# Optimization experiments

Measured on AMD Instinct MI355X. Metric: run time of the kernel, lower is better.

## Reference

```python
import jax, jax.numpy as jnp
import numpy as np

DIMS = 1024
HEAD = 16
HEAD_DIM = DIMS // HEAD  # 64
BASE_THETA = 10000.0


def setup_inputs() -> dict:
    key = jax.random.key(0)
    ks = jax.random.split(key, 8)
    B, S = 2, 2048
    x = jax.random.normal(ks[0], (B, S, DIMS), dtype=jnp.float32)
    # causal additive mask (use -1e9 instead of -inf for finite grads)
    mask = jnp.where(jnp.tril(jnp.ones((S, S), dtype=bool)), 0.0, -1e9).astype(jnp.float32)
    init = 0.02
    Wq = jax.random.normal(ks[1], (DIMS, DIMS), dtype=jnp.float32) * init
    bq = jnp.zeros((DIMS,), dtype=jnp.float32)
    Wk = jax.random.normal(ks[2], (DIMS, DIMS), dtype=jnp.float32) * init  # no bias
    Wv = jax.random.normal(ks[3], (DIMS, DIMS), dtype=jnp.float32) * init
    bv = jnp.zeros((DIMS,), dtype=jnp.float32)
    Wo = jax.random.normal(ks[4], (DIMS, DIMS), dtype=jnp.float32) * init
    bo = jnp.zeros((DIMS,), dtype=jnp.float32)
    # learned rotary frequencies, initialized exactly as the torch module
    inv_freq = (1.0 / (BASE_THETA ** (jnp.arange(0, HEAD_DIM, 2, dtype=jnp.float32) / HEAD_DIM))).astype(jnp.float32)
    return {"x": x, "mask": mask, "Wq": Wq, "bq": bq, "Wk": Wk, "Wv": Wv,
            "bv": bv, "Wo": Wo, "bo": bo, "inv_freq": inv_freq}


def _apply_rotary(x, cos, sin):
    # x: [B,H,S,D] with D == 2 * len(inv_freq); cos/sin: [S, D/2]
    xr = x.reshape(*x.shape[:-1], -1, 2)  # [B,H,S,D/2,2]
    a, b = xr[..., 0], xr[..., 1]
    ra = a * cos - b * sin
    rb = a * sin + b * cos
    return jnp.stack([ra, rb], axis=-1).reshape(x.shape)


def reference(x, mask, Wq, bq, Wk, Wv, bv, Wo, bo, inv_freq):
    B, S, D = x.shape
    H, hd = HEAD, HEAD_DIM
    q = jnp.einsum('bsd,ed->bse', x, Wq) + bq
    k = jnp.einsum('bsd,ed->bse', x, Wk)
    v = jnp.einsum('bsd,ed->bse', x, Wv) + bv
    # [B,S,D] -> [B,H,S,hd]
    q = q.reshape(B, S, H, hd).transpose(0, 2, 1, 3)
    k = k.reshape(B, S, H, hd).transpose(0, 2, 1, 3)
    v = v.reshape(B, S, H, hd).transpose(0, 2, 1, 3)
    # rotary embeddings (complex mul expressed with cos/sin)
    t = jnp.arange(S, dtype=jnp.float32)
    freqs = t[:, None] * inv_freq[None, :]  # [S, hd/2]
    cos, sin = jnp.cos(freqs), jnp.sin(freqs)
    q = _apply_rotary(q, cos, sin)
    k = _apply_rotary(k, cos, sin)
    scale = hd ** (-0.25)
    qk = jnp.einsum('bhqd,bhkd->bhqk', q * scale, k * scale)
    qk = qk + mask[:S, :S]
    qk = qk.astype(jnp.float32)
    w = jax.nn.softmax(qk, axis=-1)  # dropout is identity in eval mode
    out = jnp.einsum('bhqk,bhkd->bhqd', w, v)
    out = out.transpose(0, 2, 1, 3).reshape(B, S, D)
    out = jnp.einsum('bsd,ed->bse', out, Wo) + bo
    return (out, qk)
```

## Files before the change

kernel.cpp:

```cpp
#include <hip/hip_runtime.h>

typedef __attribute__((ext_vector_type(8))) short short8;
typedef __attribute__((ext_vector_type(4))) float floatx4;
typedef unsigned short ushort_t;

static __device__ __forceinline__ ushort_t f2bf(float f) {
  union { float f; unsigned u; } v; v.f = f;
  unsigned r = v.u + 0x7fffu + ((v.u >> 16) & 1u);
  return (ushort_t)(r >> 16);
}
static __device__ __forceinline__ float bf2f(ushort_t s) {
  union { unsigned u; float f; } v; v.u = ((unsigned)s) << 16; return v.f;
}

#define L2E 1.4426950408889634f

__global__ void conv_kernel(const float* __restrict__ src, ushort_t* __restrict__ dst, int n) {
  int i = (blockIdx.x * blockDim.x + threadIdx.x) * 4;
  if (i >= n) return;
  float4 f = *(const float4*)(src + i);
  ushort4 u;
  u.x = f2bf(f.x); u.y = f2bf(f.y); u.z = f2bf(f.z); u.w = f2bf(f.w);
  *(ushort4*)(dst + i) = u;
}

__global__ void biascat_kernel(const float* __restrict__ bq, const float* __restrict__ bv,
                               float* __restrict__ bcat) {
  int i = blockIdx.x * blockDim.x + threadIdx.x;
  float v = 0.f;
  if (i < 1024) v = bq[i];
  else if (i >= 2048) v = bv[i - 2048];
  bcat[i] = v;
}

__global__ __launch_bounds__(256) void gemm_bt(
    const ushort_t* __restrict__ A, const ushort_t* __restrict__ Bm,
    const float* __restrict__ bias, float* __restrict__ Cf,
    ushort_t* __restrict__ Cb, int M, int N, int K)
{
  __shared__ ushort_t As[128 * 72];
  __shared__ ushort_t Bs[128 * 72];
  const int tid = threadIdx.x;
  const int wave = tid >> 6, lane = tid & 63;
  const int wm = wave >> 1, wn = wave & 1;
  const int lane15 = lane & 15, quad = lane >> 4;
  const int m0 = blockIdx.y * 128, n0 = blockIdx.x * 128;
  const int lrow = tid >> 3;
  const int lcol = (tid & 7) * 8;

  floatx4 acc[4][4];
#pragma unroll
  for (int a = 0; a < 4; ++a)
#pragma unroll
    for (int b = 0; b < 4; ++b) acc[a][b] = (floatx4){0.f, 0.f, 0.f, 0.f};

  for (int k0 = 0; k0 < K; k0 += 64) {
    __syncthreads();
#pragma unroll
    for (int l = 0; l < 4; ++l) {
      int row = l * 32 + lrow;
      *(short8*)(&As[row * 72 + lcol]) = *(const short8*)(A + (size_t)(m0 + row) * K + k0 + lcol);
      *(short8*)(&Bs[row * 72 + lcol]) = *(const short8*)(Bm + (size_t)(n0 + row) * K + k0 + lcol);
    }
    __syncthreads();
#pragma unroll
    for (int ks = 0; ks < 64; ks += 32) {
      short8 af[4], bf[4];
#pragma unroll
      for (int mi = 0; mi < 4; ++mi)
        af[mi] = *(const short8*)(&As[(wm * 64 + mi * 16 + lane15) * 72 + ks + quad * 8]);
#pragma unroll
      for (int ni = 0; ni < 4; ++ni)
        bf[ni] = *(const short8*)(&Bs[(wn * 64 + ni * 16 + lane15) * 72 + ks + quad * 8]);
#pragma unroll
      for (int mi = 0; mi < 4; ++mi)
#pragma unroll
        for (int ni = 0; ni < 4; ++ni)
          acc[mi][ni] = __builtin_amdgcn_mfma_f32_16x16x32_bf16(af[mi], bf[ni], acc[mi][ni], 0, 0, 0);
    }
  }

#pragma unroll
  for (int mi = 0; mi < 4; ++mi) {
#pragma unroll
    for (int ni = 0; ni < 4; ++ni) {
      const int col = n0 + wn * 64 + ni * 16 + lane15;
      const float bv = bias ? bias[col] : 0.f;
#pragma unroll
      for (int v = 0; v < 4; ++v) {
        const int row = m0 + wm * 64 + mi * 16 + quad * 4 + v;
        const float val = acc[mi][ni][v] + bv;
        if (Cf) Cf[(size_t)row * N + col] = val;
        else    Cb[(size_t)row * N + col] = f2bf(val);
      }
    }
  }
}

__global__ void rotary_kernel(ushort_t* __restrict__ qkv, const float* __restrict__ inv_freq,
                              int colbase) {
  int tid = blockIdx.x * blockDim.x + threadIdx.x;
  int f = tid & 31;
  int h = (tid >> 5) & 15;
  int s = (tid >> 9) & 2047;
  int b = tid >> 20;
  size_t idx = (size_t)(b * 2048 + s) * 3072 + colbase + h * 64 + 2 * f;
  float ang = (float)s * inv_freq[f];
  float sn, cs;
  sincosf(ang, &sn, &cs);
  float a = bf2f(qkv[idx]);
  float bb = bf2f(qkv[idx + 1]);
  qkv[idx]     = f2bf(a * cs - bb * sn);
  qkv[idx + 1] = f2bf(a * sn + bb * cs);
}

__global__ void transpose_v_kernel(const ushort_t* __restrict__ QKV, ushort_t* __restrict__ VtG) {
  int g = blockIdx.x * blockDim.x + threadIdx.x;
  int s = g & 2047;
  int dchunk = (g >> 11) & 7;
  int bh = g >> 14;
  int b = bh >> 4, h = bh & 15;
  short8 v = *(const short8*)(QKV + (size_t)(b * 2048 + s) * 3072 + 2048 + h * 64 + dchunk * 8);
  ushort_t* dst = VtG + (size_t)bh * 64 * 2048 + (size_t)dchunk * 8 * 2048 + s;
#pragma unroll
  for (int e = 0; e < 8; ++e) dst[(size_t)e * 2048] = (ushort_t)v[e];
}

__global__ void fill_kernel(float* __restrict__ qk_out) {
  const int tile = blockIdx.x;
  const int it = tile >> 4, jt = tile & 15;
  if (jt <= it) return;
  const float4 val = {-1e9f, -1e9f, -1e9f, -1e9f};
  float* base = qk_out + (size_t)blockIdx.y * 2048 * 2048 + (size_t)it * 128 * 2048 + jt * 128;
#pragma unroll
  for (int l = 0; l < 16; ++l) {
    int idx = l * 256 + threadIdx.x;
    int row = idx >> 5, c4 = (idx & 31) * 4;
    *(float4*)(base + (size_t)row * 2048 + c4) = val;
  }
}

__global__ __launch_bounds__(256) void score_kernel(
    const ushort_t* __restrict__ QKV, float* __restrict__ qk_out,
    float2* __restrict__ pstats )
{
  const int tid = threadIdx.x;
  const int w = tid >> 6, lane = tid & 63;
  const int lane15 = lane & 15, quad = lane >> 4;
  const int t = blockIdx.x;
  const int bh = blockIdx.y;
  const int b = bh >> 4, h = bh & 15;

  int it = (int)((sqrtf((float)(8 * t + 1)) - 1.0f) * 0.5f);
  while ((it + 1) * (it + 2) / 2 <= t) ++it;
  while (it * (it + 1) / 2 > t) --it;
  const int jt = t - it * (it + 1) / 2;

  const int i_base = it * 128 + w * 32;
  const int j0 = jt * 128;
  const size_t srow0 = (size_t)b * 2048;

  short8 aq[2][2];
#pragma unroll
  for (int mi = 0; mi < 2; ++mi)
#pragma unroll
    for (int kb = 0; kb < 2; ++kb)
      aq[mi][kb] = *(const short8*)(QKV + (srow0 + i_base + mi * 16 + lane15) * 3072
                                    + h * 64 + kb * 32 + quad * 8);

  floatx4 s[2][8];
#pragma unroll
  for (int mi = 0; mi < 2; ++mi)
#pragma unroll
    for (int ni = 0; ni < 8; ++ni) s[mi][ni] = (floatx4){0.f, 0.f, 0.f, 0.f};
#pragma unroll
  for (int ni = 0; ni < 8; ++ni) {
#pragma unroll
    for (int kb = 0; kb < 2; ++kb) {
      short8 bk = *(const short8*)(QKV + (srow0 + j0 + ni * 16 + lane15) * 3072
                                   + 1024 + h * 64 + kb * 32 + quad * 8);
      s[0][ni] = __builtin_amdgcn_mfma_f32_16x16x32_bf16(aq[0][kb], bk, s[0][ni], 0, 0, 0);
      s[1][ni] = __builtin_amdgcn_mfma_f32_16x16x32_bf16(aq[1][kb], bk, s[1][ni], 0, 0, 0);
    }
  }

  float* qk_bh = qk_out + (size_t)bh * 2048 * 2048;

#pragma unroll
  for (int mi = 0; mi < 2; ++mi) {
#pragma unroll
    for (int ni = 0; ni < 8; ++ni) {
      const int j_g = j0 + ni * 16 + lane15;
#pragma unroll
      for (int v = 0; v < 4; ++v) {
        const int i_g = i_base + mi * 16 + quad * 4 + v;
        float val = s[mi][ni][v] * 0.125f + ((j_g <= i_g) ? 0.f : -1e9f);
        s[mi][ni][v] = val;
        qk_bh[(size_t)i_g * 2048 + j_g] = val;
      }
    }
  }

#pragma unroll
  for (int mi = 0; mi < 2; ++mi) {
#pragma unroll
    for (int v = 0; v < 4; ++v) {
      float mv = -3.0e38f;
#pragma unroll
      for (int ni = 0; ni < 8; ++ni) mv = fmaxf(mv, s[mi][ni][v]);
#pragma unroll
      for (int off = 1; off < 16; off <<= 1)
        mv = fmaxf(mv, __shfl_xor(mv, off));
      float ls = 0.f;
#pragma unroll
      for (int ni = 0; ni < 8; ++ni)
        ls += exp2f((s[mi][ni][v] - mv) * L2E);
#pragma unroll
      for (int off = 1; off < 16; off <<= 1)
        ls += __shfl_xor(ls, off);
      if (lane15 == 0) {
        const int i_g = i_base + mi * 16 + quad * 4 + v;
        pstats[(size_t)(bh * 2048 + i_g) * 16 + jt] = make_float2(mv, ls);
      }
    }
  }
}

__global__ void stats_kernel(const float2* __restrict__ pstats, float2* __restrict__ fstats) {
  int r = blockIdx.x * blockDim.x + threadIdx.x;
  int i = r & 2047;
  int nt = (i >> 7) + 1;
  const float2* p = pstats + (size_t)r * 16;
  float m = -3.0e38f;
  for (int t = 0; t < nt; ++t) m = fmaxf(m, p[t].x);
  float l = 0.f;
  for (int t = 0; t < nt; ++t) l += p[t].y * exp2f((p[t].x - m) * L2E);
  fstats[r] = make_float2(m, 1.f / l);
}

__global__ __launch_bounds__(256) void pv_kernel(
    const float* __restrict__ qk, const ushort_t* __restrict__ VtG,
    const float2* __restrict__ fstats, ushort_t* __restrict__ AO)
{
  const int tid = threadIdx.x;
  const int w = tid >> 6, lane = tid & 63;
  const int lane15 = lane & 15, quad = lane >> 4;
  const int wid = blockIdx.x * 4 + w;
  const int bh = wid >> 6, p = wid & 63;
  const int b = bh >> 4, h = bh & 15;

  const float* qk_bh = qk + (size_t)bh * 2048 * 2048;
  const ushort_t* Vt_bh = VtG + (size_t)bh * 64 * 2048;
  const float2* fs = fstats + (size_t)bh * 2048;

#pragma unroll
  for (int half = 0; half < 2; ++half) {
    const int s16 = half ? (127 - p) : p;
    const int i0 = s16 * 16;
    const int njt = (s16 >> 3) + 1;
    const float mr = fs[i0 + lane15].x;

    floatx4 o[4];
#pragma unroll
    for (int nd = 0; nd < 4; ++nd) o[nd] = (floatx4){0.f, 0.f, 0.f, 0.f};

    for (int jt = 0; jt < njt; ++jt) {
      const int j0 = jt * 128;
      const float* srow = qk_bh + (size_t)(i0 + lane15) * 2048 + j0 + quad * 8;

      short8 ap[4];
#pragma unroll
      for (int kb = 0; kb < 4; ++kb) {
        float4 a0 = *(const float4*)(srow + kb * 32);
        float4 a1 = *(const float4*)(srow + kb * 32 + 4);
        short8 a;
        a[0] = (short)f2bf(exp2f((a0.x - mr) * L2E));
        a[1] = (short)f2bf(exp2f((a0.y - mr) * L2E));
        a[2] = (short)f2bf(exp2f((a0.z - mr) * L2E));
        a[3] = (short)f2bf(exp2f((a0.w - mr) * L2E));
        a[4] = (short)f2bf(exp2f((a1.x - mr) * L2E));
        a[5] = (short)f2bf(exp2f((a1.y - mr) * L2E));
        a[6] = (short)f2bf(exp2f((a1.z - mr) * L2E));
        a[7] = (short)f2bf(exp2f((a1.w - mr) * L2E));
        ap[kb] = a;
      }

#pragma unroll
      for (int kb = 0; kb < 4; ++kb)
#pragma unroll
        for (int nd = 0; nd < 4; ++nd) {
          short8 bv = *(const short8*)(Vt_bh + (size_t)(nd * 16 + lane15) * 2048
                                       + j0 + kb * 32 + quad * 8);
          o[nd] = __builtin_amdgcn_mfma_f32_16x16x32_bf16(ap[kb], bv, o[nd], 0, 0, 0);
        }
    }

    float inv[4];
#pragma unroll
    for (int v = 0; v < 4; ++v) inv[v] = fs[i0 + quad * 4 + v].y;
#pragma unroll
    for (int nd = 0; nd < 4; ++nd)
#pragma unroll
      for (int v = 0; v < 4; ++v) {
        const int i_g = i0 + quad * 4 + v;
        AO[((size_t)b * 2048 + i_g) * 1024 + h * 64 + nd * 16 + lane15] =
            f2bf(o[nd][v] * inv[v]);
      }
  }
}

extern "C" void kernel_launch(void* const* d_in, const int* in_sizes, int n_in,
                              void* d_out, int out_size, void* d_ws, size_t ws_size,
                              hipStream_t stream) {
  const float* x  = (const float*)d_in[0];
  const float* Wq = (const float*)d_in[2];
  const float* bq = (const float*)d_in[3];
  const float* Wk = (const float*)d_in[4];
  const float* Wv = (const float*)d_in[5];
  const float* bv = (const float*)d_in[6];
  const float* Wo = (const float*)d_in[7];
  const float* bo = (const float*)d_in[8];
  const float* inv_freq = (const float*)d_in[9];

  char* ws = (char*)d_ws;
  ushort_t* xb   = (ushort_t*)(ws);
  ushort_t* vtg  = (ushort_t*)(ws);
  ushort_t* wb   = (ushort_t*)(ws + ((size_t)8  << 20));
  float*    bcat = (float*)   (ws + ((size_t)16 << 20));
  float2*   fstats = (float2*)(ws + ((size_t)16 << 20));
  ushort_t* qkv  = (ushort_t*)(ws + ((size_t)17 << 20));
  float2*   pstats = (float2*)(ws + ((size_t)41 << 20));
  ushort_t* aob  = (ushort_t*)(ws + ((size_t)41 << 20));

  float* out0  = (float*)d_out;
  float* qkout = out0 + 4194304;

  conv_kernel<<<4096, 256, 0, stream>>>(x, xb, 4194304);
  conv_kernel<<<1024, 256, 0, stream>>>(Wq, wb,           1048576);
  conv_kernel<<<1024, 256, 0, stream>>>(Wk, wb + 1048576, 1048576);
  conv_kernel<<<1024, 256, 0, stream>>>(Wv, wb + 2097152, 1048576);
  conv_kernel<<<1024, 256, 0, stream>>>(Wo, wb + 3145728, 1048576);
  biascat_kernel<<<12, 256, 0, stream>>>(bq, bv, bcat);

  gemm_bt<<<dim3(24, 32), 256, 0, stream>>>(xb, wb, bcat, nullptr, qkv, 4096, 3072, 1024);

  rotary_kernel<<<8192, 256, 0, stream>>>(qkv, inv_freq, 0);
  rotary_kernel<<<8192, 256, 0, stream>>>(qkv, inv_freq, 1024);

  transpose_v_kernel<<<2048, 256, 0, stream>>>(qkv, vtg);

  fill_kernel<<<dim3(256, 32), 256, 0, stream>>>(qkout);

  score_kernel<<<dim3(136, 32), 256, 0, stream>>>(qkv, qkout, pstats);

  stats_kernel<<<256, 256, 0, stream>>>(pstats, fstats);

  pv_kernel<<<512, 256, 0, stream>>>(qkout, vtg, fstats, aob);

  gemm_bt<<<dim3(8, 32), 256, 0, stream>>>(aob, wb + 3145728, bo, out0, nullptr, 4096, 1024, 1024);
}
```

Before: 949.2 us.

## Use direct global-to-LDS loads in GEMM and split PV key tiles across wave pairs

The GEMM tile loads now use global_load_lds to copy from global memory straight into LDS, dropping the register round-trip. The LDS rows lose their padding (stride 64 instead of 72), which may add bank conflicts on the MFMA fragment reads. The PV kernel now gives each row-pair to two waves that handle alternating key tiles, then combines their partial accumulators through shared memory. This doubles the launched blocks to improve occupancy and latency hiding in the memory-bound PV pass, at the cost of an LDS reduction and a block barrier.

```diff
diff --git a/kernel.cpp b/kernel.cpp
--- a/kernel.cpp
+++ b/kernel.cpp
@@ -3,6 +3,9 @@
 typedef __attribute__((ext_vector_type(8))) short short8;
 typedef __attribute__((ext_vector_type(4))) float floatx4;
 typedef unsigned short ushort_t;
+
+typedef __attribute__((address_space(1))) const ushort_t gas_ushort;
+typedef __attribute__((address_space(3))) ushort_t las_ushort;
 
 static __device__ __forceinline__ ushort_t f2bf(float f) {
   union { float f; unsigned u; } v; v.f = f;
@@ -38,15 +41,15 @@
     const float* __restrict__ bias, float* __restrict__ Cf,
     ushort_t* __restrict__ Cb, int M, int N, int K)
 {
-  __shared__ ushort_t As[128 * 72];
-  __shared__ ushort_t Bs[128 * 72];
+  __shared__ ushort_t As[128 * 64];
+  __shared__ ushort_t Bs[128 * 64];
   const int tid = threadIdx.x;
   const int wave = tid >> 6, lane = tid & 63;
   const int wm = wave >> 1, wn = wave & 1;
   const int lane15 = lane & 15, quad = lane >> 4;
   const int m0 = blockIdx.y * 128, n0 = blockIdx.x * 128;
-  const int lrow = tid >> 3;
-  const int lcol = (tid & 7) * 8;
+  const int srow = lane >> 3;
+  const int scol = (lane & 7) * 8;
 
   floatx4 acc[4][4];
 #pragma unroll
@@ -57,10 +60,15 @@
   for (int k0 = 0; k0 < K; k0 += 64) {
     __syncthreads();
 #pragma unroll
-    for (int l = 0; l < 4; ++l) {
-      int row = l * 32 + lrow;
-      *(short8*)(&As[row * 72 + lcol]) = *(const short8*)(A + (size_t)(m0 + row) * K + k0 + lcol);
-      *(short8*)(&Bs[row * 72 + lcol]) = *(const short8*)(Bm + (size_t)(n0 + row) * K + k0 + lcol);
+    for (int pc = 0; pc < 4; ++pc) {
+      const int chunk = pc * 4 + wave;
+      const int row = chunk * 8 + srow;
+      __builtin_amdgcn_global_load_lds(
+          (gas_ushort*)(A + (size_t)(m0 + row) * K + k0 + scol),
+          (las_ushort*)(As + chunk * 512 + lane * 8), 16, 0, 0);
+      __builtin_amdgcn_global_load_lds(
+          (gas_ushort*)(Bm + (size_t)(n0 + row) * K + k0 + scol),
+          (las_ushort*)(Bs + chunk * 512 + lane * 8), 16, 0, 0);
     }
     __syncthreads();
 #pragma unroll
@@ -68,10 +76,10 @@
       short8 af[4], bf[4];
 #pragma unroll
       for (int mi = 0; mi < 4; ++mi)
-        af[mi] = *(const short8*)(&As[(wm * 64 + mi * 16 + lane15) * 72 + ks + quad * 8]);
+        af[mi] = *(const short8*)(&As[(wm * 64 + mi * 16 + lane15) * 64 + ks + quad * 8]);
 #pragma unroll
       for (int ni = 0; ni < 4; ++ni)
-        bf[ni] = *(const short8*)(&Bs[(wn * 64 + ni * 16 + lane15) * 72 + ks + quad * 8]);
+        bf[ni] = *(const short8*)(&Bs[(wn * 64 + ni * 16 + lane15) * 64 + ks + quad * 8]);
 #pragma unroll
       for (int mi = 0; mi < 4; ++mi)
 #pragma unroll
@@ -242,16 +250,24 @@
     const float* __restrict__ qk, const ushort_t* __restrict__ VtG,
     const float2* __restrict__ fstats, ushort_t* __restrict__ AO)
 {
+  __shared__ float cbuf[2][2][4][64][4];
   const int tid = threadIdx.x;
   const int w = tid >> 6, lane = tid & 63;
   const int lane15 = lane & 15, quad = lane >> 4;
-  const int wid = blockIdx.x * 4 + w;
-  const int bh = wid >> 6, p = wid & 63;
+  const int pib = w >> 1, sub = w & 1;
+  const int pairId = blockIdx.x * 2 + pib;
+  const int bh = pairId >> 6, p = pairId & 63;
   const int b = bh >> 4, h = bh & 15;
 
   const float* qk_bh = qk + (size_t)bh * 2048 * 2048;
   const ushort_t* Vt_bh = VtG + (size_t)bh * 64 * 2048;
   const float2* fs = fstats + (size_t)bh * 2048;
+
+  floatx4 o[2][4];
+#pragma unroll
+  for (int half = 0; half < 2; ++half)
+#pragma unroll
+    for (int nd = 0; nd < 4; ++nd) o[half][nd] = (floatx4){0.f, 0.f, 0.f, 0.f};
 
 #pragma unroll
   for (int half = 0; half < 2; ++half) {
@@ -260,11 +276,7 @@
     const int njt = (s16 >> 3) + 1;
     const float mr = fs[i0 + lane15].x;
 
-    floatx4 o[4];
-#pragma unroll
-    for (int nd = 0; nd < 4; ++nd) o[nd] = (floatx4){0.f, 0.f, 0.f, 0.f};
-
-    for (int jt = 0; jt < njt; ++jt) {
+    for (int jt = sub; jt < njt; jt += 2) {
       const int j0 = jt * 128;
       const float* srow = qk_bh + (size_t)(i0 + lane15) * 2048 + j0 + quad * 8;
 
@@ -291,21 +303,38 @@
         for (int nd = 0; nd < 4; ++nd) {
           short8 bv = *(const short8*)(Vt_bh + (size_t)(nd * 16 + lane15) * 2048
                                        + j0 + kb * 32 + quad * 8);
-          o[nd] = __builtin_amdgcn_mfma_f32_16x16x32_bf16(ap[kb], bv, o[nd], 0, 0, 0);
+          o[half][nd] = __builtin_amdgcn_mfma_f32_16x16x32_bf16(ap[kb], bv, o[half][nd], 0, 0, 0);
         }
     }
-
-    float inv[4];
-#pragma unroll
-    for (int v = 0; v < 4; ++v) inv[v] = fs[i0 + quad * 4 + v].y;
-#pragma unroll
-    for (int nd = 0; nd < 4; ++nd)
-#pragma unroll
-      for (int v = 0; v < 4; ++v) {
-        const int i_g = i0 + quad * 4 + v;
-        AO[((size_t)b * 2048 + i_g) * 1024 + h * 64 + nd * 16 + lane15] =
-            f2bf(o[nd][v] * inv[v]);
-      }
+  }
+
+  if (sub == 1) {
+#pragma unroll
+    for (int half = 0; half < 2; ++half)
+#pragma unroll
+      for (int nd = 0; nd < 4; ++nd)
+        *(floatx4*)&cbuf[pib][half][nd][lane][0] = o[half][nd];
+  }
+  __syncthreads();
+  if (sub == 0) {
+#pragma unroll
+    for (int half = 0; half < 2; ++half) {
+      const int s16 = half ? (127 - p) : p;
+      const int i0 = s16 * 16;
+      float inv[4];
+#pragma unroll
+      for (int v = 0; v < 4; ++v) inv[v] = fs[i0 + quad * 4 + v].y;
+#pragma unroll
+      for (int nd = 0; nd < 4; ++nd) {
+        floatx4 t = *(const floatx4*)&cbuf[pib][half][nd][lane][0];
+#pragma unroll
+        for (int v = 0; v < 4; ++v) {
+          const int i_g = i0 + quad * 4 + v;
+          AO[((size_t)b * 2048 + i_g) * 1024 + h * 64 + nd * 16 + lane15] =
+              f2bf((o[half][nd][v] + t[v]) * inv[v]);
+        }
+      }
+    }
   }
 }
 
@@ -355,7 +384,7 @@
 
   stats_kernel<<<256, 256, 0, stream>>>(pstats, fstats);
 
-  pv_kernel<<<512, 256, 0, stream>>>(qkout, vtg, fstats, aob);
+  pv_kernel<<<1024, 256, 0, stream>>>(qkout, vtg, fstats, aob);
 
   gemm_bt<<<dim3(8, 32), 256, 0, stream>>>(aob, wb + 3145728, bo, out0, nullptr, 4096, 1024, 1024);
 }
```

Result: faster. 927.6 us (-2.3%).
